# Kernel tuning notes

Measured on AMD Instinct MI355X. Metric: run time of the kernel, lower is better.

## Reference

```python
import jax, jax.numpy as jnp
import numpy as np

B, L, D, NH = 4, 1500, 512, 8
HD = D // NH
EPS = 1e-8            # F.normalize eps
PEPS = 1.1920929e-07  # torch clamp_probs eps for float32
TEMP = 1.0


def setup_inputs():
    key = jax.random.key(0)
    ks = jax.random.split(key, 12)
    s = 1.0 / np.sqrt(D)
    eye = jnp.eye(D, dtype=jnp.float32)
    return {
        "hidden": jax.random.normal(ks[0], (B, L, D), jnp.float32),
        "lengths": jnp.ones((B,), jnp.float32),
        "u_noise": jax.random.uniform(ks[1], (B, L), jnp.float32),
        "W1": jax.random.normal(ks[2], (D, D), jnp.float32) * s,
        "b1": jnp.zeros((D,), jnp.float32),
        "W2": jax.random.normal(ks[3], (D, D), jnp.float32) * s,
        "b2": jnp.zeros((D,), jnp.float32),
        "Wq": eye + jax.random.normal(ks[4], (D, D), jnp.float32) * 0.01,
        "Wk": eye + jax.random.normal(ks[5], (D, D), jnp.float32) * 0.01,
        "sim_bias": jnp.float32(0.098),
        "learned_query": jax.random.normal(ks[6], (D,), jnp.float32),
        "Wpk": eye + jax.random.normal(ks[7], (D, D), jnp.float32) * 0.01,
        "Wpv": eye + jax.random.normal(ks[8], (D, D), jnp.float32) * 0.01,
        "Wpo": eye + jax.random.normal(ks[9], (D, D), jnp.float32) * 0.01,
        "ln_g": jnp.ones((D,), jnp.float32),
        "ln_b": jnp.zeros((D,), jnp.float32),
    }


def reference(hidden, lengths, u_noise, W1, b1, W2, b2, Wq, Wk, sim_bias,
              learned_query, Wpk, Wpv, Wpo, ln_g, ln_b):
    Bb, Ll, Dd = hidden.shape

    def nrm(x):
        n = jnp.sqrt(jnp.sum(x * x, -1, keepdims=True))
        return x / jnp.maximum(n, EPS)

    def mlp(x):
        return jax.nn.gelu(x @ W1.T + b1, approximate=False) @ W2.T + b2

    # boundary logits from adjacent-frame cosine similarity (dropout = eval identity)
    q_in = nrm(hidden[:, :-1]); q = nrm(mlp(q_in) + q_in) @ Wq.T
    k_in = nrm(hidden[:, 1:]);  k = nrm(mlp(k_in) + k_in) @ Wk.T
    cos = jnp.sum(q * k, -1)                                   # (B, L-1)
    probs = jnp.clip((1.0 - (cos + sim_bias)) * 0.5, 0.0, 1.0)
    probs = jnp.pad(probs, ((0, 0), (0, 1)))                   # (B, L)

    # RelaxedBernoulli rsample with explicit logistic noise
    p = jnp.clip(probs, PEPS, 1.0 - PEPS)
    u = jnp.clip(u_noise, PEPS, 1.0 - PEPS)
    soft = jax.nn.sigmoid((jnp.log(p) - jnp.log1p(-p) + jnp.log(u) - jnp.log1p(-u)) / TEMP)
    hard = (soft > 0.5).astype(hidden.dtype)

    idx = jnp.arange(Ll)
    valid_len = jnp.minimum((lengths * (Ll + 1)).astype(jnp.int32) - 1, Ll)
    trunc = (valid_len < Ll)[:, None]
    zmask = trunc & (idx[None] >= valid_len[:, None])
    omask = trunc & (idx[None] == valid_len[:, None])
    soft = jnp.where(omask, 1.0, jnp.where(zmask, 0.0, soft))
    hard = jnp.where(omask, 1.0, jnp.where(zmask, 0.0, hard))
    hard_b = hard - jax.lax.stop_gradient(soft) + soft         # straight-through
    # emergency boundary for all-zero rows
    no_b = (jnp.sum(hard, 1) == 0)[:, None]
    hard_b = jnp.where(no_b & (idx[None] == jnp.minimum(valid_len, Ll - 1)[:, None]), 1.0, hard_b)

    # segment membership (common()): token l in segment s iff exclusive cumsum == s
    seg = jnp.cumsum(hard_b, 1) - hard_b                       # (B, L)
    lmask = idx[None] < (lengths * Ll).astype(jnp.int32)[:, None]
    seg_mask = (seg[:, :, None] == idx[None, None, :].astype(hidden.dtype)) & lmask[:, :, None]  # (B,L,S)

    # layernorm + K/V projections
    mu = jnp.mean(hidden, -1, keepdims=True)
    hv = hidden - mu
    hn = hv / jnp.sqrt(jnp.mean(hv * hv, -1, keepdims=True) + 1e-5) * ln_g + ln_b
    keys = (hn @ Wpk.T).reshape(Bb, Ll, NH, HD)
    vals = (hn @ Wpv.T).reshape(Bb, Ll, NH, HD)

    # query is shared across segments -> scores only differ via the segment mask
    qh = learned_query.reshape(NH, HD)
    base = jnp.einsum('hd,blhd->bhl', qh, keys) * (HD ** -0.5)  # (B,H,L)
    mask_t = jnp.transpose(seg_mask, (0, 2, 1))[:, None]        # (B,1,S,L)
    sc = jnp.where(mask_t, base[:, :, None, :], -jnp.inf)       # (B,H,S,L)
    aw = jnp.nan_to_num(jax.nn.softmax(sc, axis=-1))            # empty segments -> 0 rows
    pooled = jnp.einsum('bhsl,blhd->bshd', aw, vals).reshape(Bb, Ll, Dd)
    return pooled @ Wpo.T                                       # (B, S=L, D)
```

## Files before the change

### kernel.cpp

```cpp
#include <hip/hip_runtime.h>
#include <math.h>

#define Bz 4
#define Lz 1500
#define Dz 512
#define NHz 8
#define Nz (Bz*Lz)
#define PEPSf 1.1920929e-07f

typedef __bf16 bf16x8 __attribute__((ext_vector_type(8)));
typedef unsigned short u16x8 __attribute__((ext_vector_type(8)));
typedef float f32x4 __attribute__((ext_vector_type(4)));
typedef unsigned short us;

__device__ __forceinline__ us f2bf(float f) {
  unsigned u = __float_as_uint(f);
  return (us)((u + 0x7fffu + ((u >> 16) & 1u)) >> 16);
}
__device__ __forceinline__ float bf2f(us b) {
  return __uint_as_float(((unsigned)b) << 16);
}
__device__ __forceinline__ int ti_idx(int row, int col) {
  return (((row >> 4) * 64 + (col >> 3)) << 7) + ((row & 15) << 3) + (col & 7);
}
__device__ __forceinline__ void st_tiled(us* __restrict__ P, int row, int col, us v) {
  P[ti_idx(row, col)] = v;
}

__device__ __forceinline__ bool decode_blk(int bx, int ncg, int& R, int& cg) {
  int xcd = bx & 7, v = bx >> 3;
  cg = v % ncg;
  R = (v / ncg) * 8 + xcd;
  return R < 94;
}

__global__ __launch_bounds__(256) void k_wconv(
    const float* __restrict__ s0, const float* __restrict__ s1, const float* __restrict__ s2,
    const float* __restrict__ s3,
    const float* __restrict__ Wq, const float* __restrict__ Wk,
    const float* __restrict__ Wpk, const float* __restrict__ lq,
    us* __restrict__ h0, us* __restrict__ h1, us* __restrict__ h2, us* __restrict__ h3,
    us* __restrict__ l0, us* __restrict__ l1,
    us* __restrict__ WkTh, us* __restrict__ WkTl, us* __restrict__ WqTh, us* __restrict__ WqTl,
    float* __restrict__ wqe) {
  const int rt = blockIdx.x, mat = blockIdx.y, t = threadIdx.x;
  if (mat == 8) {
    if (rt < 8) {
      for (int d = t; d < Dz; d += 256) {
        float acc = 0.f;
        for (int e = 0; e < 64; ++e) acc += lq[rt * 64 + e] * Wpk[(size_t)(rt * 64 + e) * Dz + d];
        wqe[rt * Dz + d] = acc;
      }
    }
    return;
  }
  const float* S; us* H; us* L = nullptr; bool tr = false;
  switch (mat) {
    case 0: S = s0; H = h0; L = l0; break;
    case 1: S = s1; H = h1; L = l1; break;
    case 2: S = s2; H = h2; break;
    case 3: S = s3; H = h3; break;
    case 4: S = Wk; H = WkTh; L = WkTl; tr = true; break;
    default: S = Wq; H = WqTh; L = WqTl; tr = true; break;
  }
  for (int e = t; e < 8192; e += 256) {
    int mm = e >> 9, c = e & 511;
    float x = tr ? S[(size_t)c * 512 + (rt * 16 + mm)]
                 : S[(size_t)(rt * 16 + mm) * 512 + c];
    us hb = f2bf(x);
    int off = ((rt * 64 + (c >> 3)) << 7) + (mm << 3) + (c & 7);
    H[off] = hb;
    if (L) L[off] = f2bf(x - bf2f(hb));
  }
}

__global__ __launch_bounds__(256) void k_rowprep(const float* __restrict__ h,
    const float* __restrict__ g, const float* __restrict__ bb,
    const float* __restrict__ wqe,
    us* __restrict__ Uh, us* __restrict__ Ul, us* __restrict__ HNh,
    float* __restrict__ base) {
  const int row = blockIdx.x;
  const int t = threadIdx.x;
  const float* x = h + (size_t)row * Dz;
  float x0 = x[t], x1 = x[t + 256];
  float s = x0 + x1, q = x0 * x0 + x1 * x1;
  #pragma unroll
  for (int o = 32; o > 0; o >>= 1) { s += __shfl_xor(s, o, 64); q += __shfl_xor(q, o, 64); }
  __shared__ float ls[4], lq[4];
  __shared__ float xs[Dz];
  if ((t & 63) == 0) { ls[t >> 6] = s; lq[t >> 6] = q; }
  __syncthreads();
  s = ls[0] + ls[1] + ls[2] + ls[3];
  q = lq[0] + lq[1] + lq[2] + lq[3];
  float un = 1.f / fmaxf(sqrtf(q), 1e-8f);
  float u0 = x0 * un, u1 = x1 * un;
  us hb0 = f2bf(u0), hb1 = f2bf(u1);
  st_tiled(Uh, row, t, hb0);       st_tiled(Ul, row, t, f2bf(u0 - bf2f(hb0)));
  st_tiled(Uh, row, t + 256, hb1); st_tiled(Ul, row, t + 256, f2bf(u1 - bf2f(hb1)));
  float mu = s * (1.f / 512.f);
  float var = fmaxf(q * (1.f / 512.f) - mu * mu, 0.f);
  float r = rsqrtf(var + 1e-5f);
  float hn0 = (x0 - mu) * r * g[t] + bb[t];
  float hn1 = (x1 - mu) * r * g[t + 256] + bb[t + 256];
  st_tiled(HNh, row, t, f2bf(hn0));
  st_tiled(HNh, row, t + 256, f2bf(hn1));
  xs[t] = hn0; xs[t + 256] = hn1;
  __syncthreads();
  const int hh = t >> 5, lane = t & 31;
  float accb = 0.f;
  for (int d = lane; d < Dz; d += 32) accb += xs[d] * wqe[hh * Dz + d];
  #pragma unroll
  for (int o = 16; o > 0; o >>= 1) accb += __shfl_xor(accb, o, 32);
  if (lane == 0) base[(size_t)row * NHz + hh] = accb * 0.125f;
}

template<int SPLIT>
__device__ __forceinline__ void gemm_body(
    const us* __restrict__ Ah, const us* __restrict__ Al,
    const us* __restrict__ Bh, const us* __restrict__ Bl,
    const float* __restrict__ bias,
    const us* __restrict__ addH, const us* __restrict__ addL, int doGelu,
    float* __restrict__ outF, us* __restrict__ outH, us* __restrict__ outL,
    int R, int cg, int colbase, int Nrows) {
  const int t = threadIdx.x, w = t >> 6, l = t & 63;
  const int m = l & 15, q = l >> 4;
  const int wr = w & 1, wc = w >> 1;
  const int laneoff = q * 128 + m * 8;
  const int nrtm1 = (Nrows >> 4) - 1;

  const u16x8* pa[2]; const u16x8* pal[2];
  const u16x8* pb[2]; const u16x8* pbl[2];
  #pragma unroll
  for (int i = 0; i < 2; ++i) {
    int rt = min(R * 4 + wr * 2 + i, nrtm1);
    pa[i] = (const u16x8*)(Ah + (size_t)rt * 8192 + laneoff);
    if (SPLIT == 3) pal[i] = (const u16x8*)(Al + (size_t)rt * 8192 + laneoff);
  }
  #pragma unroll
  for (int j = 0; j < 2; ++j) {
    int ct = cg * 4 + wc * 2 + j;
    pb[j] = (const u16x8*)(Bh + (size_t)ct * 8192 + laneoff);
    if (SPLIT == 3) pbl[j] = (const u16x8*)(Bl + (size_t)ct * 8192 + laneoff);
  }

  u16x8 bAh[2][2], bAl[2][2], bBh[2][2], bBl[2][2];
  #pragma unroll
  for (int i = 0; i < 2; ++i) {
    bAh[0][i] = pa[i][0];
    if (SPLIT == 3) bAl[0][i] = pal[i][0];
  }
  #pragma unroll
  for (int j = 0; j < 2; ++j) {
    bBh[0][j] = pb[j][0];
    if (SPLIT == 3) bBl[0][j] = pbl[j][0];
  }

  f32x4 acc[2][2];
  #pragma unroll
  for (int i = 0; i < 2; ++i)
    #pragma unroll
    for (int j = 0; j < 2; ++j) acc[i][j] = (f32x4){0.f, 0.f, 0.f, 0.f};

  #pragma unroll 2
  for (int s = 0; s < 16; ++s) {
    const int cur = s & 1, nxt = cur ^ 1;
    const int sn = (s + 1) & 15;
    #pragma unroll
    for (int i = 0; i < 2; ++i) {
      bAh[nxt][i] = pa[i][sn * 64];
      if (SPLIT == 3) bAl[nxt][i] = pal[i][sn * 64];
    }
    #pragma unroll
    for (int j = 0; j < 2; ++j) {
      bBh[nxt][j] = pb[j][sn * 64];
      if (SPLIT == 3) bBl[nxt][j] = pbl[j][sn * 64];
    }
    #pragma unroll
    for (int i = 0; i < 2; ++i)
      #pragma unroll
      for (int j = 0; j < 2; ++j) {
        bf16x8 a = __builtin_bit_cast(bf16x8, bAh[cur][i]);
        bf16x8 b = __builtin_bit_cast(bf16x8, bBh[cur][j]);
        acc[i][j] = __builtin_amdgcn_mfma_f32_16x16x32_bf16(a, b, acc[i][j], 0, 0, 0);
        if (SPLIT == 3) {
          bf16x8 al_ = __builtin_bit_cast(bf16x8, bAl[cur][i]);
          bf16x8 bl_ = __builtin_bit_cast(bf16x8, bBl[cur][j]);
          acc[i][j] = __builtin_amdgcn_mfma_f32_16x16x32_bf16(a, bl_, acc[i][j], 0, 0, 0);
          acc[i][j] = __builtin_amdgcn_mfma_f32_16x16x32_bf16(al_, b, acc[i][j], 0, 0, 0);
        }
      }
  }

  const int row0 = R * 64 + wr * 32;
  const int col0 = colbase + wc * 32;
  #pragma unroll
  for (int i = 0; i < 2; ++i) {
    #pragma unroll
    for (int r = 0; r < 4; ++r) {
      const int grow = row0 + i * 16 + q * 4 + r;
      if (grow >= Nrows) continue;
      #pragma unroll
      for (int j = 0; j < 2; ++j) {
        const int gcol = col0 + j * 16 + m;
        float v = acc[i][j][r];
        if (bias)   v += bias[gcol];
        if (addH) {
          int ai = ti_idx(grow, gcol);
          v += bf2f(addH[ai]) + bf2f(addL[ai]);
        }
        if (doGelu) v = 0.5f * v * (1.f + erff(v * 0.70710678118654752f));
        if (outF) outF[(size_t)grow * Dz + gcol] = v;
        if (outH) {
          us hb = f2bf(v);
          st_tiled(outH, grow, gcol, hb);
          if (outL) st_tiled(outL, grow, gcol, f2bf(v - bf2f(hb)));
        }
      }
    }
  }
}

__global__ __launch_bounds__(256, 4) void g_t1_vals_gt(
    const us* Uh, const us* Ul, const us* W1h, const us* W1l, const float* b1, us* T1h, us* T1l,
    const us* HNh, const us* Wpvh, float* VALS,
    const us* WkTh, const us* WkTl, const us* WqTh, const us* WqTl, us* Gth, us* Gtl) {
  if (blockIdx.z == 2) {
    int bx = blockIdx.x;
    if (bx >= 64) return;
    gemm_body<3>(WkTh, WkTl, WqTh, WqTl, nullptr, nullptr, nullptr, 0,
                 nullptr, Gth, Gtl, bx >> 3, bx & 7, (bx & 7) * 64, 512);
    return;
  }
  int R, cg;
  if (!decode_blk(blockIdx.x, 8, R, cg)) return;
  if (blockIdx.z == 0)
    gemm_body<3>(Uh, Ul, W1h, W1l, b1, nullptr, nullptr, 1,
                 nullptr, T1h, T1l, R, cg, cg * 64, Nz);
  else
    gemm_body<1>(HNh, nullptr, Wpvh, nullptr, nullptr, nullptr, nullptr, 0,
                 VALS, nullptr, nullptr, R, cg, cg * 64, Nz);
}

__global__ __launch_bounds__(256, 4) void g_w2(
    const us* T1h, const us* T1l, const us* W2h, const us* W2l, const float* b2,
    const us* Uh, const us* Ul, float* M, us* Mh, us* Ml) {
  int R, cg;
  if (!decode_blk(blockIdx.x, 8, R, cg)) return;
  gemm_body<3>(T1h, T1l, W2h, W2l, b2, Uh, Ul, 0, M, Mh, Ml, R, cg, cg * 64, Nz);
}

__global__ __launch_bounds__(256, 4) void g_p(
    const us* Mh, const us* Ml, const us* Gth, const us* Gtl, float* P) {
  int R, cg;
  if (!decode_blk(blockIdx.x, 8, R, cg)) return;
  gemm_body<3>(Mh, Ml, Gth, Gtl, nullptr, nullptr, nullptr, 0,
               P, nullptr, nullptr, R, cg, cg * 64, Nz);
}

__global__ __launch_bounds__(256, 4) void g_out(
    const us* Ph, const us* Wpoh, float* out) {
  int R, cg;
  if (!decode_blk(blockIdx.x, 8, R, cg)) return;
  gemm_body<1>(Ph, nullptr, Wpoh, nullptr, nullptr, nullptr, nullptr, 0,
               out, nullptr, nullptr, R, cg, cg * 64, Nz);
}

__global__ void k_probs(const float* __restrict__ P, const float* __restrict__ M,
                        const float* __restrict__ simb, float* __restrict__ probs) {
  const int l = blockIdx.x, b = blockIdx.y, t = threadIdx.x;
  if (l == Lz - 1) { if (t == 0) probs[(size_t)b * Lz + l] = 0.f; return; }
  const float* pp = P + ((size_t)b * Lz + l) * Dz;
  const float* m0 = M + ((size_t)b * Lz + l) * Dz;
  const float* m1 = M + ((size_t)b * Lz + l + 1) * Dz;
  float accd = 0.f, q0 = 0.f, q1 = 0.f;
  for (int i = t; i < Dz; i += 64) {
    float a = pp[i], x0 = m0[i], x1 = m1[i];
    accd += a * x1; q0 += x0 * x0; q1 += x1 * x1;
  }
  #pragma unroll
  for (int o = 32; o > 0; o >>= 1) {
    accd += __shfl_xor(accd, o, 64);
    q0 += __shfl_xor(q0, o, 64);
    q1 += __shfl_xor(q1, o, 64);
  }
  if (t == 0) {
    float un0 = 1.f / fmaxf(sqrtf(q0), 1e-8f);
    float un1 = 1.f / fmaxf(sqrtf(q1), 1e-8f);
    float cosv = accd * un0 * un1;
    float p = (1.f - (cosv + simb[0])) * 0.5f;
    probs[(size_t)b * Lz + l] = fminf(fmaxf(p, 0.f), 1.f);
  }
}

__global__ __launch_bounds__(256) void k_boundary(const float* __restrict__ probs,
    const float* __restrict__ un, const float* __restrict__ lengths,
    int* __restrict__ seg_start, int* __restrict__ seg_meta) {
  const int b = blockIdx.x, t = threadIdx.x;
  __shared__ float hard[Lz];
  __shared__ float ps[256];
  __shared__ float ws4[4];
  const float len = lengths[b];
  const int valid_len = min((int)(len * (Lz + 1)) - 1, Lz);
  const int Lm = (int)(len * Lz);
  const bool trunc = valid_len < Lz;
  for (int l = t; l < Lz; l += 256) {
    float p = probs[(size_t)b * Lz + l];
    p = fminf(fmaxf(p, PEPSf), 1.f - PEPSf);
    float u = un[(size_t)b * Lz + l];
    u = fminf(fmaxf(u, PEPSf), 1.f - PEPSf);
    float z = logf(p) - log1pf(-p) + logf(u) - log1pf(-u);
    float soft = 1.f / (1.f + expf(-z));
    float hd = soft > 0.5f ? 1.f : 0.f;
    if (trunc && l >= valid_len) hd = (l == valid_len) ? 1.f : 0.f;
    hard[l] = hd;
  }
  __syncthreads();
  float sm = 0.f;
  for (int l = t; l < Lz; l += 256) sm += hard[l];
  #pragma unroll
  for (int o = 32; o > 0; o >>= 1) sm += __shfl_xor(sm, o, 64);
  if ((t & 63) == 0) ws4[t >> 6] = sm;
  __syncthreads();
  float total = ws4[0] + ws4[1] + ws4[2] + ws4[3];
  if (total == 0.f && t == 0) hard[min(valid_len, Lz - 1)] = 1.f;
  __syncthreads();
  const int l0 = t * 6;
  float loc = 0.f;
  for (int i = 0; i < 6; ++i) { int l = l0 + i; if (l < Lz) loc += hard[l]; }
  ps[t] = loc;
  __syncthreads();
  for (int off = 1; off < 256; off <<= 1) {
    float v = (t >= off) ? ps[t - off] : 0.f;
    __syncthreads();
    ps[t] += v;
    __syncthreads();
  }
  float run = ps[t] - loc;
  for (int i = 0; i < 6; ++i) {
    int l = l0 + i; if (l >= Lz) break;
    int seg = (int)(run + 0.5f);
    if (l == 0) seg_start[b * (Lz + 1) + 0] = 0;
    else if (hard[l - 1] > 0.5f) seg_start[b * (Lz + 1) + seg] = l;
    if (l == Lz - 1) {
      int nseg = seg + 1;
      seg_meta[b * 2 + 0] = nseg;
      seg_meta[b * 2 + 1] = Lm;
      seg_start[b * (Lz + 1) + nseg] = Lz;
    }
    run += hard[l];
  }
}

__global__ __launch_bounds__(256) void k_pool(const float* __restrict__ base,
    const float* __restrict__ VALS, const int* __restrict__ seg_start,
    const int* __restrict__ seg_meta, us* __restrict__ Ph) {
  const int s = blockIdx.x, b = blockIdx.y, t = threadIdx.x;
  const int orow = b * Lz + s;
  const int nseg = seg_meta[b * 2], Lm = seg_meta[b * 2 + 1];
  int start = 0, end = 0;
  bool empty = true;
  if (s < nseg) {
    start = seg_start[b * (Lz + 1) + s];
    end = min(seg_start[b * (Lz + 1) + s + 1], Lm);
    empty = start >= end;
  }
  if (empty) { st_tiled(Ph, orow, t, 0); st_tiled(Ph, orow, t + 256, 0); return; }
  const int h = t >> 5, lane = t & 31;
  const float* bp = base + (size_t)b * Lz * NHz + h;
  float m = -1e30f;
  for (int l = start + lane; l < end; l += 32) m = fmaxf(m, bp[(size_t)l * NHz]);
  #pragma unroll
  for (int o = 16; o > 0; o >>= 1) m = fmaxf(m, __shfl_xor(m, o, 32));
  float den = 0.f;
  for (int l = start + lane; l < end; l += 32) den += expf(bp[(size_t)l * NHz] - m);
  #pragma unroll
  for (int o = 16; o > 0; o >>= 1) den += __shfl_xor(den, o, 32);
  float a0 = 0.f, a1 = 0.f;
  const float* vp = VALS + (size_t)b * Lz * Dz + h * 64 + lane;
  for (int l = start; l < end; ++l) {
    float wgt = expf(bp[(size_t)l * NHz] - m);
    a0 += wgt * vp[(size_t)l * Dz];
    a1 += wgt * vp[(size_t)l * Dz + 32];
  }
  float inv = 1.f / den;
  st_tiled(Ph, orow, h * 64 + lane, f2bf(a0 * inv));
  st_tiled(Ph, orow, h * 64 + lane + 32, f2bf(a1 * inv));
}

extern "C" void kernel_launch(void* const* d_in, const int* in_sizes, int n_in,
                              void* d_out, int out_size, void* d_ws, size_t ws_size,
                              hipStream_t stream) {
  const float* hidden  = (const float*)d_in[0];
  const float* lengths = (const float*)d_in[1];
  const float* unoise  = (const float*)d_in[2];
  const float* W1  = (const float*)d_in[3];
  const float* b1  = (const float*)d_in[4];
  const float* W2  = (const float*)d_in[5];
  const float* b2  = (const float*)d_in[6];
  const float* Wq  = (const float*)d_in[7];
  const float* Wk  = (const float*)d_in[8];
  const float* simb   = (const float*)d_in[9];
  const float* lquery = (const float*)d_in[10];
  const float* Wpk = (const float*)d_in[11];
  const float* Wpv = (const float*)d_in[12];
  const float* Wpo = (const float*)d_in[13];
  const float* lng = (const float*)d_in[14];
  const float* lnb = (const float*)d_in[15];
  float* out = (float*)d_out;

  char* p = (char*)d_ws;
  const size_t SF = (size_t)Nz * Dz * 4;
  const size_t TP = (size_t)376 * 8192 * 2;
  const size_t WP = (size_t)32 * 8192 * 2;
  float* M    = (float*)p; p += SF;
  float* PF   = (float*)p; p += SF;
  float* VALS = (float*)p; p += SF;
  us* Uh  = (us*)p; p += TP;
  us* Ul  = (us*)p; p += TP;
  us* T1h = (us*)p; p += TP;
  us* T1l = (us*)p; p += TP;
  us* Mh  = (us*)p; p += TP;
  us* Ml  = (us*)p; p += TP;
  us* HNh = (us*)p; p += TP;
  us* Ph  = (us*)p; p += TP;
  us* W1h = (us*)p; p += WP;
  us* W1l = (us*)p; p += WP;
  us* W2h = (us*)p; p += WP;
  us* W2l = (us*)p; p += WP;
  us* Wpvh = (us*)p; p += WP;
  us* Wpoh = (us*)p; p += WP;
  us* WkTh = (us*)p; p += WP;
  us* WkTl = (us*)p; p += WP;
  us* WqTh = (us*)p; p += WP;
  us* WqTl = (us*)p; p += WP;
  us* Gth  = (us*)p; p += WP;
  us* Gtl  = (us*)p; p += WP;
  float* probs  = (float*)p; p += 24064;
  float* base   = (float*)p; p += 192000;
  int* segst    = (int*)p;   p += 24064;
  int* segmeta  = (int*)p;   p += 256;
  float* wqe    = (float*)p;

  const int G8 = 8 * 12 * 8;

  k_wconv<<<dim3(32, 9), 256, 0, stream>>>(W1, W2, Wpv, Wpo, Wq, Wk, Wpk, lquery,
      W1h, W2h, Wpvh, Wpoh, W1l, W2l, WkTh, WkTl, WqTh, WqTl, wqe);
  k_rowprep<<<Nz, 256, 0, stream>>>(hidden, lng, lnb, wqe, Uh, Ul, HNh, base);
  g_t1_vals_gt<<<dim3(G8, 1, 3), 256, 0, stream>>>(Uh, Ul, W1h, W1l, b1, T1h, T1l,
      HNh, Wpvh, VALS, WkTh, WkTl, WqTh, WqTl, Gth, Gtl);
  g_w2<<<G8, 256, 0, stream>>>(T1h, T1l, W2h, W2l, b2, Uh, Ul, M, Mh, Ml);
  g_p<<<G8, 256, 0, stream>>>(Mh, Ml, Gth, Gtl, PF);
  k_probs<<<dim3(Lz, Bz), 64, 0, stream>>>(PF, M, simb, probs);
  k_boundary<<<Bz, 256, 0, stream>>>(probs, unoise, lengths, segst, segmeta);
  k_pool<<<dim3(Lz, Bz), 256, 0, stream>>>(base, VALS, segst, segmeta, Ph);
  g_out<<<G8, 256, 0, stream>>>(Ph, Wpoh, out);
}
```

Measured before the change: 234.0 us.

## Fuse row norms and adjacent dot products into GEMM epilogues, drop k_probs

Squared row norms of M are now accumulated with atomics in the g_w2 epilogue, and the dot product of the P row with the next M row is accumulated in the g_p epilogue. This removes the full float P buffer write, its reread, and the separate k_probs kernel. The cosine and probability math moves into k_boundary, with k_rowprep zeroing the accumulators. The cost is atomic traffic, extra global reads of M in g_p, and a summation order that is no longer deterministic.

```diff
diff --git a/kernel.cpp b/kernel.cpp
--- a/kernel.cpp
+++ b/kernel.cpp
@@ -78,9 +78,10 @@
     const float* __restrict__ g, const float* __restrict__ bb,
     const float* __restrict__ wqe,
     us* __restrict__ Uh, us* __restrict__ Ul, us* __restrict__ HNh,
-    float* __restrict__ base) {
+    float* __restrict__ base, float* __restrict__ qn, float* __restrict__ dot) {
   const int row = blockIdx.x;
   const int t = threadIdx.x;
+  if (t == 0) { qn[row] = 0.f; dot[row] = 0.f; }
   const float* x = h + (size_t)row * Dz;
   float x0 = x[t], x1 = x[t + 256];
   float s = x0 + x1, q = x0 * x0 + x1 * x1;
@@ -121,6 +122,7 @@
     const float* __restrict__ bias,
     const us* __restrict__ addH, const us* __restrict__ addL, int doGelu,
     float* __restrict__ outF, us* __restrict__ outH, us* __restrict__ outL,
+    float* __restrict__ qnAcc, const float* __restrict__ Mnext, float* __restrict__ dotAcc,
     int R, int cg, int colbase, int Nrows) {
   const int t = threadIdx.x, w = t >> 6, l = t & 63;
   const int m = l & 15, q = l >> 4;
@@ -199,6 +201,7 @@
     for (int r = 0; r < 4; ++r) {
       const int grow = row0 + i * 16 + q * 4 + r;
       if (grow >= Nrows) continue;
+      float vv[2];
       #pragma unroll
       for (int j = 0; j < 2; ++j) {
         const int gcol = col0 + j * 16 + m;
@@ -209,12 +212,26 @@
           v += bf2f(addH[ai]) + bf2f(addL[ai]);
         }
         if (doGelu) v = 0.5f * v * (1.f + erff(v * 0.70710678118654752f));
+        vv[j] = v;
         if (outF) outF[(size_t)grow * Dz + gcol] = v;
         if (outH) {
           us hb = f2bf(v);
           st_tiled(outH, grow, gcol, hb);
           if (outL) st_tiled(outL, grow, gcol, f2bf(v - bf2f(hb)));
         }
+      }
+      if (qnAcc) {
+        float part = vv[0] * vv[0] + vv[1] * vv[1];
+        #pragma unroll
+        for (int o = 1; o < 16; o <<= 1) part += __shfl_xor(part, o, 64);
+        if (m == 0) atomicAdd(&qnAcc[grow], part);
+      }
+      if (dotAcc && (grow + 1) < Nrows) {
+        const float* mn = Mnext + (size_t)(grow + 1) * Dz;
+        float part = vv[0] * mn[col0 + m] + vv[1] * mn[col0 + 16 + m];
+        #pragma unroll
+        for (int o = 1; o < 16; o <<= 1) part += __shfl_xor(part, o, 64);
+        if (m == 0) atomicAdd(&dotAcc[grow], part);
       }
     }
   }
@@ -228,33 +245,36 @@
     int bx = blockIdx.x;
     if (bx >= 64) return;
     gemm_body<3>(WkTh, WkTl, WqTh, WqTl, nullptr, nullptr, nullptr, 0,
-                 nullptr, Gth, Gtl, bx >> 3, bx & 7, (bx & 7) * 64, 512);
+                 nullptr, Gth, Gtl, nullptr, nullptr, nullptr,
+                 bx >> 3, bx & 7, (bx & 7) * 64, 512);
     return;
   }
   int R, cg;
   if (!decode_blk(blockIdx.x, 8, R, cg)) return;
   if (blockIdx.z == 0)
     gemm_body<3>(Uh, Ul, W1h, W1l, b1, nullptr, nullptr, 1,
-                 nullptr, T1h, T1l, R, cg, cg * 64, Nz);
+                 nullptr, T1h, T1l, nullptr, nullptr, nullptr, R, cg, cg * 64, Nz);
   else
     gemm_body<1>(HNh, nullptr, Wpvh, nullptr, nullptr, nullptr, nullptr, 0,
-                 VALS, nullptr, nullptr, R, cg, cg * 64, Nz);
+                 VALS, nullptr, nullptr, nullptr, nullptr, nullptr, R, cg, cg * 64, Nz);
 }
 
 __global__ __launch_bounds__(256, 4) void g_w2(
     const us* T1h, const us* T1l, const us* W2h, const us* W2l, const float* b2,
-    const us* Uh, const us* Ul, float* M, us* Mh, us* Ml) {
+    const us* Uh, const us* Ul, float* M, us* Mh, us* Ml, float* qn) {
   int R, cg;
   if (!decode_blk(blockIdx.x, 8, R, cg)) return;
-  gemm_body<3>(T1h, T1l, W2h, W2l, b2, Uh, Ul, 0, M, Mh, Ml, R, cg, cg * 64, Nz);
+  gemm_body<3>(T1h, T1l, W2h, W2l, b2, Uh, Ul, 0, M, Mh, Ml, qn, nullptr, nullptr,
+               R, cg, cg * 64, Nz);
 }
 
 __global__ __launch_bounds__(256, 4) void g_p(
-    const us* Mh, const us* Ml, const us* Gth, const us* Gtl, float* P) {
+    const us* Mh, const us* Ml, const us* Gth, const us* Gtl,
+    const float* M, float* dot) {
   int R, cg;
   if (!decode_blk(blockIdx.x, 8, R, cg)) return;
   gemm_body<3>(Mh, Ml, Gth, Gtl, nullptr, nullptr, nullptr, 0,
-               P, nullptr, nullptr, R, cg, cg * 64, Nz);
+               nullptr, nullptr, nullptr, nullptr, M, dot, R, cg, cg * 64, Nz);
 }
 
 __global__ __launch_bounds__(256, 4) void g_out(
@@ -262,37 +282,11 @@
   int R, cg;
   if (!decode_blk(blockIdx.x, 8, R, cg)) return;
   gemm_body<1>(Ph, nullptr, Wpoh, nullptr, nullptr, nullptr, nullptr, 0,
-               out, nullptr, nullptr, R, cg, cg * 64, Nz);
-}
-
-__global__ void k_probs(const float* __restrict__ P, const float* __restrict__ M,
-                        const float* __restrict__ simb, float* __restrict__ probs) {
-  const int l = blockIdx.x, b = blockIdx.y, t = threadIdx.x;
-  if (l == Lz - 1) { if (t == 0) probs[(size_t)b * Lz + l] = 0.f; return; }
-  const float* pp = P + ((size_t)b * Lz + l) * Dz;
-  const float* m0 = M + ((size_t)b * Lz + l) * Dz;
-  const float* m1 = M + ((size_t)b * Lz + l + 1) * Dz;
-  float accd = 0.f, q0 = 0.f, q1 = 0.f;
-  for (int i = t; i < Dz; i += 64) {
-    float a = pp[i], x0 = m0[i], x1 = m1[i];
-    accd += a * x1; q0 += x0 * x0; q1 += x1 * x1;
-  }
-  #pragma unroll
-  for (int o = 32; o > 0; o >>= 1) {
-    accd += __shfl_xor(accd, o, 64);
-    q0 += __shfl_xor(q0, o, 64);
-    q1 += __shfl_xor(q1, o, 64);
-  }
-  if (t == 0) {
-    float un0 = 1.f / fmaxf(sqrtf(q0), 1e-8f);
-    float un1 = 1.f / fmaxf(sqrtf(q1), 1e-8f);
-    float cosv = accd * un0 * un1;
-    float p = (1.f - (cosv + simb[0])) * 0.5f;
-    probs[(size_t)b * Lz + l] = fminf(fmaxf(p, 0.f), 1.f);
-  }
-}
-
-__global__ __launch_bounds__(256) void k_boundary(const float* __restrict__ probs,
+               out, nullptr, nullptr, nullptr, nullptr, nullptr, R, cg, cg * 64, Nz);
+}
+
+__global__ __launch_bounds__(256) void k_boundary(const float* __restrict__ dot,
+    const float* __restrict__ qn, const float* __restrict__ simb,
     const float* __restrict__ un, const float* __restrict__ lengths,
     int* __restrict__ seg_start, int* __restrict__ seg_meta) {
   const int b = blockIdx.x, t = threadIdx.x;
@@ -303,9 +297,17 @@
   const int valid_len = min((int)(len * (Lz + 1)) - 1, Lz);
   const int Lm = (int)(len * Lz);
   const bool trunc = valid_len < Lz;
+  const float sb = simb[0];
   for (int l = t; l < Lz; l += 256) {
-    float p = probs[(size_t)b * Lz + l];
-    p = fminf(fmaxf(p, PEPSf), 1.f - PEPSf);
+    float pr = 0.f;
+    if (l != Lz - 1) {
+      const int row = b * Lz + l;
+      float un0 = 1.f / fmaxf(sqrtf(qn[row]), 1e-8f);
+      float un1 = 1.f / fmaxf(sqrtf(qn[row + 1]), 1e-8f);
+      float cosv = dot[row] * un0 * un1;
+      pr = fminf(fmaxf((1.f - (cosv + sb)) * 0.5f, 0.f), 1.f);
+    }
+    float p = fminf(fmaxf(pr, PEPSf), 1.f - PEPSf);
     float u = un[(size_t)b * Lz + l];
     u = fminf(fmaxf(u, PEPSf), 1.f - PEPSf);
     float z = logf(p) - log1pf(-p) + logf(u) - log1pf(-u);
@@ -413,7 +415,6 @@
   const size_t TP = (size_t)376 * 8192 * 2;
   const size_t WP = (size_t)32 * 8192 * 2;
   float* M    = (float*)p; p += SF;
-  float* PF   = (float*)p; p += SF;
   float* VALS = (float*)p; p += SF;
   us* Uh  = (us*)p; p += TP;
   us* Ul  = (us*)p; p += TP;
@@ -435,7 +436,8 @@
   us* WqTl = (us*)p; p += WP;
   us* Gth  = (us*)p; p += WP;
   us* Gtl  = (us*)p; p += WP;
-  float* probs  = (float*)p; p += 24064;
+  float* qn     = (float*)p; p += 24064;
+  float* dot    = (float*)p; p += 24064;
   float* base   = (float*)p; p += 192000;
   int* segst    = (int*)p;   p += 24064;
   int* segmeta  = (int*)p;   p += 256;
@@ -445,13 +447,12 @@
 
   k_wconv<<<dim3(32, 9), 256, 0, stream>>>(W1, W2, Wpv, Wpo, Wq, Wk, Wpk, lquery,
       W1h, W2h, Wpvh, Wpoh, W1l, W2l, WkTh, WkTl, WqTh, WqTl, wqe);
-  k_rowprep<<<Nz, 256, 0, stream>>>(hidden, lng, lnb, wqe, Uh, Ul, HNh, base);
+  k_rowprep<<<Nz, 256, 0, stream>>>(hidden, lng, lnb, wqe, Uh, Ul, HNh, base, qn, dot);
   g_t1_vals_gt<<<dim3(G8, 1, 3), 256, 0, stream>>>(Uh, Ul, W1h, W1l, b1, T1h, T1l,
       HNh, Wpvh, VALS, WkTh, WkTl, WqTh, WqTl, Gth, Gtl);
-  g_w2<<<G8, 256, 0, stream>>>(T1h, T1l, W2h, W2l, b2, Uh, Ul, M, Mh, Ml);
-  g_p<<<G8, 256, 0, stream>>>(Mh, Ml, Gth, Gtl, PF);
-  k_probs<<<dim3(Lz, Bz), 64, 0, stream>>>(PF, M, simb, probs);
-  k_boundary<<<Bz, 256, 0, stream>>>(probs, unoise, lengths, segst, segmeta);
+  g_w2<<<G8, 256, 0, stream>>>(T1h, T1l, W2h, W2l, b2, Uh, Ul, M, Mh, Ml, qn);
+  g_p<<<G8, 256, 0, stream>>>(Mh, Ml, Gth, Gtl, M, dot);
+  k_boundary<<<Bz, 256, 0, stream>>>(dot, qn, simb, unoise, lengths, segst, segmeta);
   k_pool<<<dim3(Lz, Bz), 256, 0, stream>>>(base, VALS, segst, segmeta, Ph);
   g_out<<<G8, 256, 0, stream>>>(Ph, Wpoh, out);
 }
```

After: 238.0 us. No clear change (+1.7%).
